# Kernel tuning notes

Measured on AMD Instinct MI355X. Metric: run time of the kernel, lower is better.

The kernel has to match this reference:

```python
import jax, jax.numpy as jnp
import numpy as np

K = 8          # circulant block size
H = 16         # heads


def circ_linear(x, w, b):
    """Block-circulant linear. x: [..., in], w: [p, q, K] (first column of each
    KxK circulant block), b: [p*K]. y[p] = sum_q circ(w[p,q]) @ x_block[q],
    computed as circular convolution via rFFT."""
    q = w.shape[1]
    xb = x.reshape(x.shape[:-1] + (q, K))            # [..., q, K]
    Fx = jnp.fft.rfft(xb, axis=-1)                    # [..., q, K//2+1]
    Fw = jnp.fft.rfft(w, axis=-1)                     # [p, q, K//2+1]
    Fy = jnp.einsum('pqf,...qf->...pf', Fw, Fx)
    y = jnp.fft.irfft(Fy, n=K, axis=-1)               # [..., p, K]
    return y.reshape(x.shape[:-1] + (-1,)) + b


def setup_inputs() -> dict:
    key = jax.random.key(0)
    ks = jax.random.split(key, 9)
    B, N, D = 2, 1024, 1024
    p = q = D // K
    std = 1.0 / np.sqrt(D)
    mk = lambda k: jax.random.normal(k, (p, q, K), dtype=jnp.float32) * std
    mb = lambda k: jax.random.normal(k, (D,), dtype=jnp.float32) * 0.01
    x = jax.random.normal(ks[0], (B, N, D), dtype=jnp.float32)
    # causal mask: True = masked out
    mask = (~jnp.tril(jnp.ones((N, N), dtype=bool)))[None, None]  # [1,1,N,N]
    return {
        'x': x, 'mask': mask,
        'wq': mk(ks[1]), 'bq': mb(ks[2]),
        'wk': mk(ks[3]), 'bk': mb(ks[4]),
        'wv': mk(ks[5]), 'bv': mb(ks[6]),
        'wo': mk(ks[7]), 'bo': mb(ks[8]),
    }


def reference(x, mask, wq, bq, wk, bk, wv, bv, wo, bo):
    B, N, D = x.shape
    dh = D // H
    heads = lambda a: a.reshape(B, N, H, dh).transpose(0, 2, 1, 3)  # [B,H,N,dh]
    qh = heads(circ_linear(x, wq, bq))
    kh = heads(circ_linear(x, wk, bk))
    vh = heads(circ_linear(x, wv, bv))
    attn = jnp.einsum('bhnd,bhmd->bhnm', qh, kh)
    attn = jnp.where(mask, -jnp.inf, attn)
    probs = jax.nn.softmax(attn / jnp.sqrt(jnp.float32(dh)), axis=-1)
    out = jnp.einsum('bhnm,bhmd->bhnd', probs, vh)
    out = out.transpose(0, 2, 1, 3).reshape(B, N, D)
    return circ_linear(out, wo, bo)
```

## Files before the change

### kernel.cpp

```cpp
#include <hip/hip_runtime.h>
#include <hip/hip_bf16.h>

#define DIM   1024
#define NSEQ  1024
#define BATCH 2
#define NHEAD 16
#define DH    64

typedef unsigned short u16;
typedef __attribute__((ext_vector_type(8))) short  short8;
typedef __attribute__((ext_vector_type(4))) float  f32x4;
typedef __attribute__((ext_vector_type(8))) unsigned short u16x8;
typedef __attribute__((ext_vector_type(4))) unsigned short u16x4;

#define EXP_SCALE 0.18033688011112042f
#define SLOT 4352

__device__ __forceinline__ u16 f2bf(float f) {
  union { float f; unsigned u; } v; v.f = f;
  unsigned r = v.u + 0x7FFFu + ((v.u >> 16) & 1u);
  return (u16)(r >> 16);
}

#define GLD(src, dst)                                                          \
  __builtin_amdgcn_global_load_lds(                                           \
      (const __attribute__((address_space(1))) void*)(src),                   \
      (__attribute__((address_space(3))) void*)(dst), 16, 0, 0)

__global__ __launch_bounds__(256) void prep_bf16(
    const float* __restrict__ wq, const float* __restrict__ wk,
    const float* __restrict__ wv, const float* __restrict__ wo,
    const float* __restrict__ x,
    u16* __restrict__ Wd, u16* __restrict__ Xb) {
  const int bid = blockIdx.x;
  if (bid < 2048) {
    const int z = bid >> 9;
    const float* w = (z == 0) ? wq : (z == 1) ? wk : (z == 2) ? wv : wo;
    u16* out = Wd + (size_t)z * DIM * DIM;
    const int idx8 = (bid & 511) * 256 + threadIdx.x;
    const int r = idx8 >> 7;
    const int q = idx8 & 127;
    const int p = r >> 3, a = r & 7;
    const float* wrow = w + (size_t)(p * 128 + q) * 8;
    const float4 w0 = *(const float4*)(wrow);
    const float4 w1 = *(const float4*)(wrow + 4);
    const float wv8[8] = {w0.x, w0.y, w0.z, w0.w, w1.x, w1.y, w1.z, w1.w};
    u16x8 o;
#pragma unroll
    for (int j = 0; j < 8; ++j) o[j] = f2bf(wv8[(a - j) & 7]);
    ((u16x8*)out)[idx8] = o;
  } else {
    const int i = (bid - 2048) * 256 + threadIdx.x;
    const float4 a = ((const float4*)x)[2 * i];
    const float4 b = ((const float4*)x)[2 * i + 1];
    u16x8 o;
    o[0] = f2bf(a.x); o[1] = f2bf(a.y); o[2] = f2bf(a.z); o[3] = f2bf(a.w);
    o[4] = f2bf(b.x); o[5] = f2bf(b.y); o[6] = f2bf(b.z); o[7] = f2bf(b.w);
    ((u16x8*)Xb)[i] = o;
  }
}

__global__ __launch_bounds__(256, 2) void gemm_qkv(
    const u16* __restrict__ A, const u16* __restrict__ Wd,
    const float* __restrict__ bq, const float* __restrict__ bk,
    const float* __restrict__ bv,
    u16* __restrict__ Qb, u16* __restrict__ Kb, u16* __restrict__ Vt) {
  __shared__ u16 As[2][64 * 32];
  __shared__ u16 Bs[2][3 * 64 * 32];

  const int tid  = threadIdx.x;
  const int w    = tid >> 6, lane = tid & 63;
  const int nb   = blockIdx.x * 64;
  const int mb   = blockIdx.y * 64;

  f32x4 acc[3][2][2] = {};

  const int m0 = (w >> 1) * 32, n0 = (w & 1) * 32;
  const int lr = lane & 15, lk = (lane >> 4) * 8;

  const int srow = w * 16 + (lane >> 2), skc = (lane & 3) * 8;
  const u16* Ap = A + (size_t)(mb + srow) * DIM + skc;
  const u16* Wp = Wd + (size_t)(nb + srow) * DIM + skc;

#define STAGE(buf, k0)                                                         \
  do {                                                                         \
    GLD(Ap + (k0), As[buf] + w * 512);                                         \
    _Pragma("unroll")                                                          \
    for (int i = 0; i < 3; ++i)                                                \
      GLD(Wp + (size_t)i * DIM * DIM + (k0), Bs[buf] + (i * 4 + w) * 512);     \
  } while (0)

  STAGE(0, 0);
  __syncthreads();
  int cur = 0;
  for (int k0 = 0; k0 < DIM; k0 += 32) {
    if (k0 + 32 < DIM) STAGE(cur ^ 1, k0 + 32);

    short8 a[2], b[3][2];
#pragma unroll
    for (int mi = 0; mi < 2; ++mi)
      a[mi] = *(const short8*)&As[cur][(m0 + mi * 16 + lr) * 32 + lk];
#pragma unroll
    for (int z = 0; z < 3; ++z)
#pragma unroll
      for (int ni = 0; ni < 2; ++ni)
        b[z][ni] = *(const short8*)
            &Bs[cur][z * 2048 + (n0 + ni * 16 + lr) * 32 + lk];
#pragma unroll
    for (int z = 0; z < 3; ++z)
#pragma unroll
      for (int mi = 0; mi < 2; ++mi)
#pragma unroll
        for (int ni = 0; ni < 2; ++ni)
          acc[z][mi][ni] = __builtin_amdgcn_mfma_f32_16x16x32_bf16(
              a[mi], b[z][ni], acc[z][mi][ni], 0, 0, 0);

    __syncthreads();
    cur ^= 1;
  }
#undef STAGE

  const int col = lane & 15, rq4 = (lane >> 4) * 4;

#pragma unroll
  for (int z = 0; z < 2; ++z) {
    u16* C = z ? Kb : Qb;
    const float* bias = z ? bk : bq;
#pragma unroll
    for (int ni = 0; ni < 2; ++ni) {
      const int gc = nb + n0 + ni * 16 + col;
      const float bb = bias[gc];
#pragma unroll
      for (int mi = 0; mi < 2; ++mi) {
        const size_t rbase = (size_t)(mb + m0 + mi * 16 + rq4) * DIM + gc;
#pragma unroll
        for (int j = 0; j < 4; ++j)
          C[rbase + (size_t)j * DIM] = f2bf(acc[z][mi][ni][j] + bb);
      }
    }
  }
  {
    const int b = mb >> 10;
    const int h = blockIdx.x;
    const int nbase = (mb & (NSEQ - 1)) + m0;
#pragma unroll
    for (int ni = 0; ni < 2; ++ni) {
      const int dh = n0 + ni * 16 + col;
      const float bb = bv[nb + dh];
      u16* vrow = Vt + ((size_t)(b * NHEAD + h) * DH + dh) * NSEQ;
#pragma unroll
      for (int mi = 0; mi < 2; ++mi) {
        const int nn = nbase + mi * 16 + rq4;
        u16x4 o;
#pragma unroll
        for (int j = 0; j < 4; ++j) o[j] = f2bf(acc[2][mi][ni][j] + bb);
        *(u16x4*)(vrow + nn) = o;
      }
    }
  }
}

template <int BM, int BN, int BFOUT>
__global__ __launch_bounds__(256) void gemm_bf16_nt(
    const u16* __restrict__ A, const u16* __restrict__ Wbase,
    const float* __restrict__ b0,
    void* __restrict__ C0) {
  constexpr int MR = BM / 32, NR = BN / 32;
  constexpr int CA = BM / 64, CB = BN / 64;

  const u16* W      = Wbase;
  const float* bias = b0;
  void* C           = C0;

  __shared__ u16 As[2][BM * 32];
  __shared__ u16 Bs[2][BN * 32];

  const int tid  = threadIdx.x;
  const int w    = tid >> 6, lane = tid & 63;
  const int mb   = blockIdx.y * BM, nb = blockIdx.x * BN;

  f32x4 acc[MR][NR] = {};

  const int m0 = (w >> 1) * (BM / 2), n0 = (w & 1) * (BN / 2);
  const int lr = lane & 15, lk = (lane >> 4) * 8;

  const int srow = lane >> 2, skc = (lane & 3) * 8;

#define STAGE(buf, k0)                                                         \
  do {                                                                         \
    _Pragma("unroll")                                                          \
    for (int i = 0; i < CA; ++i) {                                             \
      const int cb = w * CA + i;                                               \
      GLD(A + (size_t)(mb + cb * 16 + srow) * DIM + (k0) + skc,                \
          As[buf] + cb * 512);                                                 \
    }                                                                          \
    _Pragma("unroll")                                                          \
    for (int i = 0; i < CB; ++i) {                                             \
      const int cb = w * CB + i;                                               \
      GLD(W + (size_t)(nb + cb * 16 + srow) * DIM + (k0) + skc,                \
          Bs[buf] + cb * 512);                                                 \
    }                                                                          \
  } while (0)

  STAGE(0, 0);
  __syncthreads();
  int cur = 0;
  for (int k0 = 0; k0 < DIM; k0 += 32) {
    if (k0 + 32 < DIM) STAGE(cur ^ 1, k0 + 32);

    short8 a[MR], b[NR];
#pragma unroll
    for (int mi = 0; mi < MR; ++mi)
      a[mi] = *(const short8*)&As[cur][(m0 + mi * 16 + lr) * 32 + lk];
#pragma unroll
    for (int ni = 0; ni < NR; ++ni)
      b[ni] = *(const short8*)&Bs[cur][(n0 + ni * 16 + lr) * 32 + lk];
#pragma unroll
    for (int mi = 0; mi < MR; ++mi)
#pragma unroll
      for (int ni = 0; ni < NR; ++ni)
        acc[mi][ni] = __builtin_amdgcn_mfma_f32_16x16x32_bf16(
            a[mi], b[ni], acc[mi][ni], 0, 0, 0);

    __syncthreads();
    cur ^= 1;
  }
#undef STAGE

  const int col = lane & 15, rq = (lane >> 4) * 4;
#pragma unroll
  for (int ni = 0; ni < NR; ++ni) {
    const int gc = nb + n0 + ni * 16 + col;
    const float bv = bias[gc];
#pragma unroll
    for (int mi = 0; mi < MR; ++mi) {
      const size_t rbase = (size_t)(mb + m0 + mi * 16 + rq) * DIM + gc;
#pragma unroll
      for (int j = 0; j < 4; ++j) {
        const float v = acc[mi][ni][j] + bv;
        if (BFOUT) ((u16*)C)[rbase + (size_t)j * DIM] = f2bf(v);
        else       ((float*)C)[rbase + (size_t)j * DIM] = v;
      }
    }
  }
}

__global__ __launch_bounds__(256, 4) void attn_split(
    const u16* __restrict__ Qg, const u16* __restrict__ Kg,
    const u16* __restrict__ Vt, float* __restrict__ Part,
    u16* __restrict__ AOb) {
  int idx = blockIdx.x, qt = 0, cc = 0;
  for (int t = 15; t >= 0; --t) {
    const int nc = (t >> 2) + 1;
    if (idx < nc) { qt = t; cc = idx; break; }
    idx -= nc;
  }
  const int h = blockIdx.y, b = blockIdx.z;
  const int tid = threadIdx.x;
  const int w  = tid >> 6, l = tid & 63;
  const int lr = l & 15, lg = l >> 4;

  __shared__ u16 Klds[4][64 * 64];
  __shared__ u16 Vlds[4][64 * 64];
  __shared__ u16 Plds[4][16 * 64];

  const int qg = qt * 64 + w * 16 + lr;
  const size_t base_bh = (size_t)b * NSEQ * DIM + (size_t)h * DH;
  const size_t vt_bh   = (size_t)(b * NHEAD + h) * DH * NSEQ;

  short8 qf[2];
#pragma unroll
  for (int c = 0; c < 2; ++c)
    qf[c] = *(const short8*)(Qg + base_bh + (size_t)qg * DIM + c * 32 + lg * 8);

  f32x4 acc_o[4] = {};
  float m_run = -1e30f, l_run = 0.f;
  char* pbase = (char*)Plds[w];
  const int psw = (lr & 7) << 4;

  const int srow8 = l >> 3;
  const int sj    = l & 7;

  const int kt0 = cc * 4;
  const int nt  = min(kt0 + 4, qt + 1) - kt0;

#pragma unroll
  for (int t = 0; t < 4; ++t) {
    if (t < nt) {
      const int kt = kt0 + t;
#pragma unroll
      for (int i = 0; i < 2; ++i) {
        const int cb  = w * 2 + i;
        const int row = cb * 8 + srow8;
        const int c16 = sj ^ (row & 7);
        GLD(Kg + base_bh + (size_t)(kt * 64 + row) * DIM + c16 * 8,
            Klds[t] + cb * 512);
        GLD(Vt + vt_bh + (size_t)row * NSEQ + kt * 64 + c16 * 8,
            Vlds[t] + cb * 512);
      }
    }
  }
  __syncthreads();

  for (int it = 0; it < nt; ++it) {
    const int kt = kt0 + it;

    f32x4 s[4] = {};
#pragma unroll
    for (int t16 = 0; t16 < 4; ++t16) {
      const int row = t16 * 16 + lr;
#pragma unroll
      for (int c = 0; c < 2; ++c) {
        const int c16 = (c * 4 + lg) ^ (row & 7);
        const short8 kf = *(const short8*)
            ((const char*)Klds[it] + row * 128 + c16 * 16);
        s[t16] = __builtin_amdgcn_mfma_f32_16x16x32_bf16(kf, qf[c], s[t16], 0, 0, 0);
      }
    }

    const bool diag = (kt == qt);
    float mloc = -1e30f;
#pragma unroll
    for (int t16 = 0; t16 < 4; ++t16)
#pragma unroll
      for (int j = 0; j < 4; ++j) {
        float v = s[t16][j];
        if (diag && (kt * 64 + t16 * 16 + lg * 4 + j) > qg) v = -1e30f;
        s[t16][j] = v;
        mloc = fmaxf(mloc, v);
      }
    mloc = fmaxf(mloc, __shfl_xor(mloc, 16));
    mloc = fmaxf(mloc, __shfl_xor(mloc, 32));
    const float m_new = fmaxf(m_run, mloc);
    const float a = exp2f((m_run - m_new) * EXP_SCALE);
    float psum = 0.f;
    u16x4 pk[4];
#pragma unroll
    for (int t16 = 0; t16 < 4; ++t16)
#pragma unroll
      for (int j = 0; j < 4; ++j) {
        const float p = exp2f((s[t16][j] - m_new) * EXP_SCALE);
        psum += p;
        pk[t16][j] = f2bf(p);
      }
    psum += __shfl_xor(psum, 16);
    psum += __shfl_xor(psum, 32);
    l_run = l_run * a + psum;
    m_run = m_new;
#pragma unroll
    for (int d = 0; d < 4; ++d) acc_o[d] *= a;

#pragma unroll
    for (int t16 = 0; t16 < 4; ++t16)
      *(u16x4*)(pbase + lr * 128 + ((t16 * 32 + lg * 8) ^ psw)) = pk[t16];

#pragma unroll
    for (int c = 0; c < 2; ++c) {
      const short8 pf = *(const short8*)
          (pbase + lr * 128 + ((c * 64 + lg * 16) ^ psw));
#pragma unroll
      for (int d = 0; d < 4; ++d) {
        const int dh = d * 16 + lr;
        const int c16 = (c * 4 + lg) ^ (dh & 7);
        const short8 vf = *(const short8*)
            ((const char*)Vlds[it] + dh * 128 + c16 * 16);
        acc_o[d] = __builtin_amdgcn_mfma_f32_16x16x32_bf16(vf, pf, acc_o[d], 0, 0, 0);
      }
    }
  }

  const int ql = w * 16 + lr;
  if (qt < 4) {
    const float inv = 1.f / l_run;
    u16* Op = AOb + (size_t)(b * NSEQ + qt * 64 + ql) * DIM + (size_t)h * DH;
#pragma unroll
    for (int d = 0; d < 4; ++d) {
      u16x4 o;
      o[0] = f2bf(acc_o[d][0] * inv); o[1] = f2bf(acc_o[d][1] * inv);
      o[2] = f2bf(acc_o[d][2] * inv); o[3] = f2bf(acc_o[d][3] * inv);
      *(u16x4*)(Op + d * 16 + lg * 4) = o;
    }
  } else {
    float* slot = Part + (((size_t)(b * NHEAD + h) * 16 + qt) * 4 + cc) * SLOT;
#pragma unroll
    for (int d = 0; d < 4; ++d)
      *(f32x4*)(slot + ql * 64 + d * 16 + lg * 4) = acc_o[d];
    if (lg == 0) {
      slot[4096 + ql] = m_run;
      slot[4160 + ql] = l_run;
    }
  }
}

__global__ __launch_bounds__(256) void attn_merge(
    const float* __restrict__ Part, u16* __restrict__ AOb) {
  const int qt = blockIdx.x + 4, h = blockIdx.y, b = blockIdx.z;
  const int t = threadIdx.x;
  const int q = t >> 2, quad = t & 3;
  const int nc = (qt >> 2) + 1;
  const float* base = Part + ((size_t)(b * NHEAD + h) * 16 + qt) * 4 * SLOT;

  float mv[4], lv[4];
  float M = -1e30f;
  for (int c = 0; c < nc; ++c) {
    mv[c] = base[c * SLOT + 4096 + q];
    lv[c] = base[c * SLOT + 4160 + q];
    M = fmaxf(M, mv[c]);
  }
  float L = 0.f, fc[4];
  for (int c = 0; c < nc; ++c) {
    fc[c] = exp2f((mv[c] - M) * EXP_SCALE);
    L += lv[c] * fc[c];
  }
  const float inv = 1.f / L;

  float o[16] = {};
  for (int c = 0; c < nc; ++c) {
    const float* op = base + c * SLOT + q * 64 + quad * 16;
    const float f = fc[c];
#pragma unroll
    for (int i = 0; i < 4; ++i) {
      const f32x4 v = *(const f32x4*)(op + i * 4);
      o[i * 4 + 0] += f * v[0]; o[i * 4 + 1] += f * v[1];
      o[i * 4 + 2] += f * v[2]; o[i * 4 + 3] += f * v[3];
    }
  }

  u16* dst = AOb + (size_t)(b * NSEQ + qt * 64 + q) * DIM + h * DH + quad * 16;
  u16x8 o0, o1;
#pragma unroll
  for (int i = 0; i < 8; ++i) { o0[i] = f2bf(o[i] * inv); o1[i] = f2bf(o[8 + i] * inv); }
  *(u16x8*)(dst)     = o0;
  *(u16x8*)(dst + 8) = o1;
}

extern "C" void kernel_launch(void* const* d_in, const int* in_sizes, int n_in,
                              void* d_out, int out_size, void* d_ws, size_t ws_size,
                              hipStream_t stream) {
  const float* x  = (const float*)d_in[0];
  const float* wq = (const float*)d_in[2];
  const float* bq = (const float*)d_in[3];
  const float* wk = (const float*)d_in[4];
  const float* bk = (const float*)d_in[5];
  const float* wv = (const float*)d_in[6];
  const float* bv = (const float*)d_in[7];
  const float* wo = (const float*)d_in[8];
  const float* bo = (const float*)d_in[9];

  char* ws = (char*)d_ws;
  u16* Wd    = (u16*)(ws);
  u16* Xb    = (u16*)(ws + ((size_t)8  << 20));
  u16* Qb    = (u16*)(ws + ((size_t)12 << 20));
  u16* Kb    = (u16*)(ws + ((size_t)16 << 20));
  u16* Vt    = (u16*)(ws + ((size_t)24 << 20));
  u16* AOb   = (u16*)(ws + ((size_t)28 << 20));
  float* Prt = (float*)(ws + ((size_t)32 << 20));

  prep_bf16<<<dim3(3072, 1, 1), 256, 0, stream>>>(wq, wk, wv, wo, x, Wd, Xb);

  gemm_qkv<<<dim3(NHEAD, (BATCH * NSEQ) / 64, 1), 256, 0, stream>>>(
      Xb, Wd, bq, bk, bv, Qb, Kb, Vt);

  attn_split<<<dim3(40, NHEAD, BATCH), 256, 0, stream>>>(Qb, Kb, Vt, Prt, AOb);

  attn_merge<<<dim3(12, NHEAD, BATCH), 256, 0, stream>>>(Prt, AOb);

  gemm_bf16_nt<64, 64, 0><<<dim3(DIM / 64, (BATCH * NSEQ) / 64, 1), 256, 0, stream>>>(
      AOb, Wd + (size_t)3 * DIM * DIM, bo, d_out);
}
```

Before: 83.26 us.

## Double-buffer K/V tiles and fuse split-KV merge via atomic counter

Attention now splits KV work into chunks of up to 8 tiles instead of 4, so at most 2 chunks per query tile and 24 blocks per head instead of 40. K/V tiles are double-buffered in LDS and prefetched one step ahead, replacing the old up-front load of all tiles. The separate merge kernel is removed: the second block to finish a query tile, detected with an atomic counter, merges the partial results itself. MFMA sections also get raised wave priority. This cuts a kernel launch and LDS footprint but adds a per-iteration barrier, a memset, threadfence traffic, and fewer blocks, so less parallelism.

```diff
diff --git a/kernel.cpp b/kernel.cpp
--- a/kernel.cpp
+++ b/kernel.cpp
@@ -248,20 +248,18 @@
 __global__ __launch_bounds__(256, 4) void attn_split(
     const u16* __restrict__ Qg, const u16* __restrict__ Kg,
     const u16* __restrict__ Vt, float* __restrict__ Part,
-    u16* __restrict__ AOb) {
-  int idx = blockIdx.x, qt = 0, cc = 0;
-  for (int t = 15; t >= 0; --t) {
-    const int nc = (t >> 2) + 1;
-    if (idx < nc) { qt = t; cc = idx; break; }
-    idx -= nc;
-  }
+    int* __restrict__ Cnt, u16* __restrict__ AOb) {
+  const int x = blockIdx.x;
+  int qt, cc;
+  if (x < 16) { qt = 15 - (x >> 1); cc = x & 1; }
+  else        { qt = 23 - x;        cc = 0;     }
   const int h = blockIdx.y, b = blockIdx.z;
   const int tid = threadIdx.x;
   const int w  = tid >> 6, l = tid & 63;
   const int lr = l & 15, lg = l >> 4;
 
-  __shared__ u16 Klds[4][64 * 64];
-  __shared__ u16 Vlds[4][64 * 64];
+  __shared__ u16 Klds[2][64 * 64];
+  __shared__ u16 Vlds[2][64 * 64];
   __shared__ u16 Plds[4][16 * 64];
 
   const int qg = qt * 64 + w * 16 + lr;
@@ -281,31 +279,33 @@
   const int srow8 = l >> 3;
   const int sj    = l & 7;
 
-  const int kt0 = cc * 4;
-  const int nt  = min(kt0 + 4, qt + 1) - kt0;
-
-#pragma unroll
-  for (int t = 0; t < 4; ++t) {
-    if (t < nt) {
-      const int kt = kt0 + t;
-#pragma unroll
-      for (int i = 0; i < 2; ++i) {
-        const int cb  = w * 2 + i;
-        const int row = cb * 8 + srow8;
-        const int c16 = sj ^ (row & 7);
-        GLD(Kg + base_bh + (size_t)(kt * 64 + row) * DIM + c16 * 8,
-            Klds[t] + cb * 512);
-        GLD(Vt + vt_bh + (size_t)row * NSEQ + kt * 64 + c16 * 8,
-            Vlds[t] + cb * 512);
-      }
-    }
-  }
+#define ASTAGE(buf, kt)                                                        \
+  do {                                                                         \
+    _Pragma("unroll")                                                          \
+    for (int i = 0; i < 2; ++i) {                                              \
+      const int cb  = w * 2 + i;                                               \
+      const int row = cb * 8 + srow8;                                          \
+      const int c16 = sj ^ (row & 7);                                          \
+      GLD(Kg + base_bh + (size_t)((kt) * 64 + row) * DIM + c16 * 8,            \
+          Klds[buf] + cb * 512);                                               \
+      GLD(Vt + vt_bh + (size_t)row * NSEQ + (kt) * 64 + c16 * 8,               \
+          Vlds[buf] + cb * 512);                                               \
+    }                                                                          \
+  } while (0)
+
+  const int kt0 = cc * 8;
+  const int nt  = min(kt0 + 8, qt + 1) - kt0;
+
+  ASTAGE(0, kt0);
   __syncthreads();
+  int cur = 0;
 
   for (int it = 0; it < nt; ++it) {
     const int kt = kt0 + it;
+    if (it + 1 < nt) ASTAGE(cur ^ 1, kt + 1);
 
     f32x4 s[4] = {};
+    __builtin_amdgcn_s_setprio(1);
 #pragma unroll
     for (int t16 = 0; t16 < 4; ++t16) {
       const int row = t16 * 16 + lr;
@@ -313,10 +313,11 @@
       for (int c = 0; c < 2; ++c) {
         const int c16 = (c * 4 + lg) ^ (row & 7);
         const short8 kf = *(const short8*)
-            ((const char*)Klds[it] + row * 128 + c16 * 16);
+            ((const char*)Klds[cur] + row * 128 + c16 * 16);
         s[t16] = __builtin_amdgcn_mfma_f32_16x16x32_bf16(kf, qf[c], s[t16], 0, 0, 0);
       }
     }
+    __builtin_amdgcn_s_setprio(0);
 
     const bool diag = (kt == qt);
     float mloc = -1e30f;
@@ -354,6 +355,7 @@
     for (int t16 = 0; t16 < 4; ++t16)
       *(u16x4*)(pbase + lr * 128 + ((t16 * 32 + lg * 8) ^ psw)) = pk[t16];
 
+    __builtin_amdgcn_s_setprio(1);
 #pragma unroll
     for (int c = 0; c < 2; ++c) {
       const short8 pf = *(const short8*)
@@ -363,14 +365,19 @@
         const int dh = d * 16 + lr;
         const int c16 = (c * 4 + lg) ^ (dh & 7);
         const short8 vf = *(const short8*)
-            ((const char*)Vlds[it] + dh * 128 + c16 * 16);
+            ((const char*)Vlds[cur] + dh * 128 + c16 * 16);
         acc_o[d] = __builtin_amdgcn_mfma_f32_16x16x32_bf16(vf, pf, acc_o[d], 0, 0, 0);
       }
     }
-  }
+    __builtin_amdgcn_s_setprio(0);
+
+    __syncthreads();
+    cur ^= 1;
+  }
+#undef ASTAGE
 
   const int ql = w * 16 + lr;
-  if (qt < 4) {
+  if (qt < 8) {
     const float inv = 1.f / l_run;
     u16* Op = AOb + (size_t)(b * NSEQ + qt * 64 + ql) * DIM + (size_t)h * DH;
 #pragma unroll
@@ -380,58 +387,43 @@
       o[2] = f2bf(acc_o[d][2] * inv); o[3] = f2bf(acc_o[d][3] * inv);
       *(u16x4*)(Op + d * 16 + lg * 4) = o;
     }
-  } else {
-    float* slot = Part + (((size_t)(b * NHEAD + h) * 16 + qt) * 4 + cc) * SLOT;
-#pragma unroll
-    for (int d = 0; d < 4; ++d)
-      *(f32x4*)(slot + ql * 64 + d * 16 + lg * 4) = acc_o[d];
-    if (lg == 0) {
-      slot[4096 + ql] = m_run;
-      slot[4160 + ql] = l_run;
-    }
-  }
-}
-
-__global__ __launch_bounds__(256) void attn_merge(
-    const float* __restrict__ Part, u16* __restrict__ AOb) {
-  const int qt = blockIdx.x + 4, h = blockIdx.y, b = blockIdx.z;
-  const int t = threadIdx.x;
-  const int q = t >> 2, quad = t & 3;
-  const int nc = (qt >> 2) + 1;
-  const float* base = Part + ((size_t)(b * NHEAD + h) * 16 + qt) * 4 * SLOT;
-
-  float mv[4], lv[4];
-  float M = -1e30f;
-  for (int c = 0; c < nc; ++c) {
-    mv[c] = base[c * SLOT + 4096 + q];
-    lv[c] = base[c * SLOT + 4160 + q];
-    M = fmaxf(M, mv[c]);
-  }
-  float L = 0.f, fc[4];
-  for (int c = 0; c < nc; ++c) {
-    fc[c] = exp2f((mv[c] - M) * EXP_SCALE);
-    L += lv[c] * fc[c];
-  }
-  const float inv = 1.f / L;
-
-  float o[16] = {};
-  for (int c = 0; c < nc; ++c) {
-    const float* op = base + c * SLOT + q * 64 + quad * 16;
-    const float f = fc[c];
-#pragma unroll
-    for (int i = 0; i < 4; ++i) {
-      const f32x4 v = *(const f32x4*)(op + i * 4);
-      o[i * 4 + 0] += f * v[0]; o[i * 4 + 1] += f * v[1];
-      o[i * 4 + 2] += f * v[2]; o[i * 4 + 3] += f * v[3];
-    }
-  }
-
-  u16* dst = AOb + (size_t)(b * NSEQ + qt * 64 + q) * DIM + h * DH + quad * 16;
-  u16x8 o0, o1;
-#pragma unroll
-  for (int i = 0; i < 8; ++i) { o0[i] = f2bf(o[i] * inv); o1[i] = f2bf(o[8 + i] * inv); }
-  *(u16x8*)(dst)     = o0;
-  *(u16x8*)(dst + 8) = o1;
+    return;
+  }
+
+  const size_t pidx = ((size_t)(b * NHEAD + h) * 16 + qt) * 2;
+  float* slot = Part + (pidx + cc) * SLOT;
+#pragma unroll
+  for (int d = 0; d < 4; ++d)
+    *(f32x4*)(slot + ql * 64 + d * 16 + lg * 4) = acc_o[d];
+  if (lg == 0) {
+    slot[4096 + ql] = m_run;
+    slot[4160 + ql] = l_run;
+  }
+  __threadfence();
+  __syncthreads();
+  int* flag = (int*)&Plds[0][0];
+  if (tid == 0)
+    *flag = (atomicAdd(&Cnt[(b * NHEAD + h) * 16 + qt], 1) == 1);
+  __syncthreads();
+  if (!*flag) return;
+  __threadfence();
+
+  const float* os = Part + (pidx + (cc ^ 1)) * SLOT;
+  const float m1 = os[4096 + ql], l1 = os[4160 + ql];
+  const float M  = fmaxf(m_run, m1);
+  const float f0 = exp2f((m_run - M) * EXP_SCALE);
+  const float f1 = exp2f((m1 - M) * EXP_SCALE);
+  const float inv = 1.f / (l_run * f0 + l1 * f1);
+  u16* Op = AOb + (size_t)(b * NSEQ + qt * 64 + ql) * DIM + (size_t)h * DH;
+#pragma unroll
+  for (int d = 0; d < 4; ++d) {
+    const f32x4 o1 = *(const f32x4*)(os + ql * 64 + d * 16 + lg * 4);
+    u16x4 o;
+#pragma unroll
+    for (int j = 0; j < 4; ++j)
+      o[j] = f2bf((acc_o[d][j] * f0 + o1[j] * f1) * inv);
+    *(u16x4*)(Op + d * 16 + lg * 4) = o;
+  }
 }
 
 extern "C" void kernel_launch(void* const* d_in, const int* in_sizes, int n_in,
@@ -455,15 +447,17 @@
   u16* Vt    = (u16*)(ws + ((size_t)24 << 20));
   u16* AOb   = (u16*)(ws + ((size_t)28 << 20));
   float* Prt = (float*)(ws + ((size_t)32 << 20));
+  int*  Cnt  = (int*)(ws + ((size_t)52 << 20));
+
+  hipMemsetAsync(Cnt, 0, 512 * sizeof(int), stream);
 
   prep_bf16<<<dim3(3072, 1, 1), 256, 0, stream>>>(wq, wk, wv, wo, x, Wd, Xb);
 
   gemm_qkv<<<dim3(NHEAD, (BATCH * NSEQ) / 64, 1), 256, 0, stream>>>(
       Xb, Wd, bq, bk, bv, Qb, Kb, Vt);
 
-  attn_split<<<dim3(40, NHEAD, BATCH), 256, 0, stream>>>(Qb, Kb, Vt, Prt, AOb);
-
-  attn_merge<<<dim3(12, NHEAD, BATCH), 256, 0, stream>>>(Prt, AOb);
+  attn_split<<<dim3(24, NHEAD, BATCH), 256, 0, stream>>>(
+      Qb, Kb, Vt, Prt, Cnt, AOb);
 
   gemm_bf16_nt<64, 64, 0><<<dim3(DIM / 64, (BATCH * NSEQ) / 64, 1), 256, 0, stream>>>(
       AOb, Wd + (size_t)3 * DIM * DIM, bo, d_out);
```

Measured after the change: 186.8 us. +124.3%, slower.
